# Kernel tuning notes

Measured on AMD Instinct MI355X. Metric: run time of the kernel, lower is better.

Reference implementation:

```python
import jax, jax.numpy as jnp
import numpy as np

T, B, D, A = 512, 64, 1024, 128
NL = 2
AIN = A + 2 * D        # adapt LSTM input size: adapt + x + alstm hidden
PSZ = 2 * D + 12 * D   # policy size per layer (bias=True): ninp+nhid + 12*nhid


def setup_inputs() -> dict:
    key = jax.random.key(0)
    ks = jax.random.split(key, 12)
    r = lambda k, s: jax.random.normal(k, s, dtype=jnp.float32) * 0.03
    return {
        "x": jax.random.normal(ks[0], (T, B, D), dtype=jnp.float32),
        # layer 0
        "a_wih0": r(ks[1], (4 * A, AIN)), "a_whh0": r(ks[2], (4 * A, A)),
        "a_bih0": jnp.zeros((4 * A,), jnp.float32), "a_bhh0": jnp.zeros((4 * A,), jnp.float32),
        "p_w0": r(ks[3], (PSZ, A)), "p_b0": jnp.ones((PSZ,), jnp.float32),
        "f_wih0": r(ks[4], (4 * D, D)), "f_whh0": r(ks[5], (4 * D, D)),
        "f_b0": jnp.zeros((4 * D,), jnp.float32),
        # layer 1
        "a_wih1": r(ks[6], (4 * A, AIN)), "a_whh1": r(ks[7], (4 * A, A)),
        "a_bih1": jnp.zeros((4 * A,), jnp.float32), "a_bhh1": jnp.zeros((4 * A,), jnp.float32),
        "p_w1": r(ks[8], (PSZ, A)), "p_b1": jnp.ones((PSZ,), jnp.float32),
        "f_wih1": r(ks[9], (4 * D, D)), "f_whh1": r(ks[10], (4 * D, D)),
        "f_b1": jnp.zeros((4 * D,), jnp.float32),
    }


def _lstm_cell(x, h, c, wih, whh, bih, bhh):
    g = x @ wih.T + bih + h @ whh.T + bhh      # [B, 4A]
    i, f, gg, o = jnp.split(g, 4, axis=1)
    c2 = jax.nn.sigmoid(f) * c + jax.nn.sigmoid(i) * jnp.tanh(gg)
    h2 = jax.nn.sigmoid(o) * jnp.tanh(c2)
    return h2, c2


def _alstm_cell(xt, h, c, pol, wih, whh, b):
    # policy chunks: [ninp, nhid, 4n, 4n, 4n] with ninp=nhid=D
    p0 = pol[:, :D]
    p1 = pol[:, D:2 * D]
    p2 = pol[:, 2 * D:6 * D]
    p3 = pol[:, 6 * D:10 * D]
    p4 = pol[:, 10 * D:14 * D]
    ig = ((xt * p0) @ wih.T) * p2 + b * p4
    hg = ((h * p1) @ whh.T) * p3
    g = ig + hg
    i, f, gg, o = jnp.split(g, 4, axis=1)
    c2 = jax.nn.sigmoid(f) * c + jax.nn.sigmoid(i) * jnp.tanh(gg)
    h2 = jax.nn.sigmoid(o) * jnp.tanh(c2)
    return h2, c2


def reference(x, a_wih0, a_whh0, a_bih0, a_bhh0, p_w0, p_b0, f_wih0, f_whh0, f_b0,
              a_wih1, a_whh1, a_bih1, a_bhh1, p_w1, p_b1, f_wih1, f_whh1, f_b1):
    params = [
        (a_wih0, a_whh0, a_bih0, a_bhh0, p_w0, p_b0, f_wih0, f_whh0, f_b0),
        (a_wih1, a_whh1, a_bih1, a_bhh1, p_w1, p_b1, f_wih1, f_whh1, f_b1),
    ]

    def step(carry, xt):
        ah, ac, fh, fc = (list(t) for t in carry)
        xc = xt
        for l in range(NL):
            awih, awhh, abih, abhh, pw, pb, fwih, fwhh, fb = params[l]
            # nlayers != 1: adapt input = [x, alstm hidden, prev-layer adapt hidden]
            # (Python negative indexing at l=0 picks last layer's adapt hidden from t-1,
            #  matching the torch in-place list update semantics.)
            ax = jnp.concatenate([xc, fh[l], ah[l - 1]], axis=1)
            ah[l], ac[l] = _lstm_cell(ax, ah[l], ac[l], awih, awhh, abih, abhh)
            pol = ah[l] @ pw.T + pb                      # Project: Linear(A -> PSZ)
            fh[l], fc[l] = _alstm_cell(xc, fh[l], fc[l], pol, fwih, fwhh, fb)
            xc = fh[l]
        return (tuple(ah), tuple(ac), tuple(fh), tuple(fc)), xc

    za = jnp.zeros((B, A), x.dtype)
    zf = jnp.zeros((B, D), x.dtype)
    carry0 = ((za,) * NL, (za,) * NL, (zf,) * NL, (zf,) * NL)
    _, ys = jax.lax.scan(step, carry0, x)   # [T, B, D]
    return ys
```

## Files before the change

kernel.cpp:

```cpp
#include <hip/hip_runtime.h>

#define T_ 512
#define B_ 64
#define D_ 1024
#define A_ 128
#define KCAT_ 2304
#define PSZ_ 14336

typedef __attribute__((ext_vector_type(8))) short short8;
typedef __attribute__((ext_vector_type(4))) short short4_t;
typedef __attribute__((ext_vector_type(4))) float float4_t;

__device__ __forceinline__ float sigf(float x){ return 1.0f/(1.0f + __expf(-x)); }
__device__ __forceinline__ float tanhf_(float x){ return 2.0f/(1.0f + __expf(-2.0f*x)) - 1.0f; }

__device__ __forceinline__ short f2bf(float f){
  unsigned u = __builtin_bit_cast(unsigned, f);
  u += 0x7fffu + ((u >> 16) & 1u);
  return (short)(u >> 16);
}
__device__ __forceinline__ float bf2f(short s){
  unsigned u = ((unsigned)(unsigned short)s) << 16;
  return __builtin_bit_cast(float, u);
}

__global__ __launch_bounds__(256) void pk_cat(const float* __restrict__ wih,
                                              const float* __restrict__ whh,
                                              short* __restrict__ dst){
  int c = blockIdx.x*256 + threadIdx.x;
  int n = blockIdx.y;
  if (c >= KCAT_) return;
  float v = (c < 2176) ? wih[(size_t)n*2176 + c] : whh[n*A_ + (c - 2176)];
  dst[(size_t)n*KCAT_ + c] = f2bf(v);
}
__global__ __launch_bounds__(256) void pk_conv(const float* __restrict__ src,
                                               short* __restrict__ dst, int n){
  int i = blockIdx.x*256 + threadIdx.x;
  if (i < n) dst[i] = f2bf(src[i]);
}

__global__ __launch_bounds__(64) void k1_gates(
    const short* __restrict__ Wcat,
    const float* __restrict__ xf,
    const short* __restrict__ xbf,
    const short* __restrict__ fhbf,
    const short* __restrict__ ahp,
    const short* __restrict__ ahs,
    const float* __restrict__ bih, const float* __restrict__ bhh,
    float* __restrict__ gates)
{
  const int lane = threadIdx.x;
  const int mt = blockIdx.x >> 2, nt = blockIdx.x & 3;
  const int row = lane & 15, quad = lane >> 4;
  const int m0 = mt*16;
  const short* wrow = Wcat + (size_t)(m0 + row)*KCAT_ + quad*8;
  const int bq = nt*16 + row;
  float4_t acc = {0.f,0.f,0.f,0.f};

  if (xf){
    const float* xp = xf + (size_t)bq*D_ + quad*8;
    #pragma unroll 4
    for (int ks = 0; ks < 32; ++ks){
      short8 a = *(const short8*)(wrow + ks*32);
      float4_t x0 = *(const float4_t*)(xp + ks*32);
      float4_t x1 = *(const float4_t*)(xp + ks*32 + 4);
      short8 bfr;
      #pragma unroll
      for (int i = 0; i < 4; ++i){ bfr[i] = f2bf(x0[i]); bfr[4+i] = f2bf(x1[i]); }
      acc = __builtin_amdgcn_mfma_f32_16x16x32_bf16(a, bfr, acc, 0, 0, 0);
    }
  } else {
    const short* xp = xbf + (size_t)bq*D_ + quad*8;
    #pragma unroll 4
    for (int ks = 0; ks < 32; ++ks){
      short8 a = *(const short8*)(wrow + ks*32);
      short8 bfr = *(const short8*)(xp + ks*32);
      acc = __builtin_amdgcn_mfma_f32_16x16x32_bf16(a, bfr, acc, 0, 0, 0);
    }
  }
  {
    const short* hp = fhbf + (size_t)bq*D_ + quad*8;
    #pragma unroll 4
    for (int ks = 0; ks < 32; ++ks){
      short8 a = *(const short8*)(wrow + 1024 + ks*32);
      short8 bfr = *(const short8*)(hp + ks*32);
      acc = __builtin_amdgcn_mfma_f32_16x16x32_bf16(a, bfr, acc, 0, 0, 0);
    }
  }
  {
    const short* pp = ahp + bq*A_ + quad*8;
    #pragma unroll
    for (int ks = 0; ks < 4; ++ks){
      short8 a = *(const short8*)(wrow + 2048 + ks*32);
      short8 bfr = *(const short8*)(pp + ks*32);
      acc = __builtin_amdgcn_mfma_f32_16x16x32_bf16(a, bfr, acc, 0, 0, 0);
    }
  }
  {
    const short* sp = ahs + bq*A_ + quad*8;
    #pragma unroll
    for (int ks = 0; ks < 4; ++ks){
      short8 a = *(const short8*)(wrow + 2176 + ks*32);
      short8 bfr = *(const short8*)(sp + ks*32);
      acc = __builtin_amdgcn_mfma_f32_16x16x32_bf16(a, bfr, acc, 0, 0, 0);
    }
  }
  const int b = nt*16 + row;
  const int n0 = m0 + quad*4;
  #pragma unroll
  for (int r = 0; r < 4; ++r){
    int n = n0 + r;
    gates[n*B_ + b] = acc[r] + bih[n] + bhh[n];
  }
}

__global__ __launch_bounds__(256) void k2_cellpol(
    const float* __restrict__ gates,
    const float* __restrict__ ac_old, float* __restrict__ ac_new,
    short* __restrict__ ah_out,
    const short* __restrict__ pwbf,
    const float* __restrict__ pb,
    const float* __restrict__ xf,
    const short* __restrict__ xbf,
    const short* __restrict__ fhbf,
    float* __restrict__ polp,
    short* __restrict__ xp0, short* __restrict__ hp1)
{
  __shared__ short ah_s[64*136];
  const int tid = threadIdx.x;
  const int b = tid & 63, q = tid >> 6;
  for (int jj = 0; jj < 32; ++jj){
    int j = q*32 + jj;
    float gi = gates[(j      )*B_ + b];
    float gf = gates[(j + 128)*B_ + b];
    float gg = gates[(j + 256)*B_ + b];
    float go = gates[(j + 384)*B_ + b];
    float c  = ac_old[j*B_ + b];
    float c2 = sigf(gf)*c + sigf(gi)*tanhf_(gg);
    float h2 = sigf(go)*tanhf_(c2);
    ah_s[b*136 + j] = f2bf(h2);
    if (blockIdx.x == 0){
      ac_new[j*B_ + b] = c2;
      ah_out[b*A_ + j] = f2bf(h2);
    }
  }
  __syncthreads();
  const int lane = tid & 63;
  const int row = lane & 15, quad = lane >> 4;
  const int m0 = (blockIdx.x*4 + q)*16;
  const short* wrow = pwbf + (size_t)(m0 + row)*A_ + quad*8;
  float4_t acc[4] = {{0.f,0.f,0.f,0.f},{0.f,0.f,0.f,0.f},{0.f,0.f,0.f,0.f},{0.f,0.f,0.f,0.f}};
  #pragma unroll
  for (int ks = 0; ks < 4; ++ks){
    short8 a = *(const short8*)(wrow + ks*32);
    #pragma unroll
    for (int nt = 0; nt < 4; ++nt){
      short8 bf8 = *(const short8*)&ah_s[(nt*16 + row)*136 + ks*32 + quad*8];
      acc[nt] = __builtin_amdgcn_mfma_f32_16x16x32_bf16(a, bf8, acc[nt], 0, 0, 0);
    }
  }
  const int c0 = m0 + quad*4;
  float4_t pbv = *(const float4_t*)(pb + c0);
  if (m0 < 1024){
    #pragma unroll
    for (int nt = 0; nt < 4; ++nt){
      int b2 = nt*16 + row;
      float4_t xv;
      if (xf){ xv = *(const float4_t*)(xf + (size_t)b2*D_ + c0); }
      else {
        short4_t xb = *(const short4_t*)(xbf + (size_t)b2*D_ + c0);
        #pragma unroll
        for (int r = 0; r < 4; ++r) xv[r] = bf2f(xb[r]);
      }
      short4_t o;
      #pragma unroll
      for (int r = 0; r < 4; ++r) o[r] = f2bf((acc[nt][r] + pbv[r]) * xv[r]);
      *(short4_t*)(xp0 + (size_t)b2*D_ + c0) = o;
    }
  } else if (m0 < 2048){
    int cc = c0 - 1024;
    #pragma unroll
    for (int nt = 0; nt < 4; ++nt){
      int b2 = nt*16 + row;
      short4_t hb = *(const short4_t*)(fhbf + (size_t)b2*D_ + cc);
      short4_t o;
      #pragma unroll
      for (int r = 0; r < 4; ++r) o[r] = f2bf((acc[nt][r] + pbv[r]) * bf2f(hb[r]));
      *(short4_t*)(hp1 + (size_t)b2*D_ + cc) = o;
    }
  } else {
    int cc = c0 - 2048;
    #pragma unroll
    for (int nt = 0; nt < 4; ++nt){
      int b2 = nt*16 + row;
      float4_t vv;
      #pragma unroll
      for (int r = 0; r < 4; ++r) vv[r] = acc[nt][r] + pbv[r];
      *(float4_t*)(polp + (size_t)b2*12288 + cc) = vv;
    }
  }
}

__global__ __launch_bounds__(256) void k3_fast(
    const short* __restrict__ wI,
    const short* __restrict__ wH,
    const short* __restrict__ xp0, const short* __restrict__ hp1,
    const float* __restrict__ polp,
    const float* __restrict__ fb,
    float* __restrict__ fc,
    short* __restrict__ fhbf,
    float* __restrict__ outp)
{
  const int tid = threadIdx.x;
  const int lane = tid & 63, nt = tid >> 6;
  const int row = lane & 15, quad = lane >> 4;
  const int j0 = blockIdx.x*16;
  const short* wIr[4]; const short* wHr[4];
  #pragma unroll
  for (int g = 0; g < 4; ++g){
    wIr[g] = wI + (size_t)(g*D_ + j0 + row)*D_ + quad*8;
    wHr[g] = wH + (size_t)(g*D_ + j0 + row)*D_ + quad*8;
  }
  const short* bx = xp0 + (size_t)(nt*16 + row)*D_ + quad*8;
  const short* bh = hp1 + (size_t)(nt*16 + row)*D_ + quad*8;
  float4_t aI[4] = {{0.f,0.f,0.f,0.f},{0.f,0.f,0.f,0.f},{0.f,0.f,0.f,0.f},{0.f,0.f,0.f,0.f}};
  float4_t aH[4] = {{0.f,0.f,0.f,0.f},{0.f,0.f,0.f,0.f},{0.f,0.f,0.f,0.f},{0.f,0.f,0.f,0.f}};
  #pragma unroll 2
  for (int ks = 0; ks < 32; ++ks){
    const int kg = ks*32;
    short8 bxf = *(const short8*)(bx + kg);
    short8 bhf = *(const short8*)(bh + kg);
    #pragma unroll
    for (int g = 0; g < 4; ++g){
      short8 ai = *(const short8*)(wIr[g] + kg);
      short8 ah = *(const short8*)(wHr[g] + kg);
      aI[g] = __builtin_amdgcn_mfma_f32_16x16x32_bf16(ai, bxf, aI[g], 0, 0, 0);
      aH[g] = __builtin_amdgcn_mfma_f32_16x16x32_bf16(ah, bhf, aH[g], 0, 0, 0);
    }
  }
  const int b = nt*16 + row;
  const int jr = j0 + quad*4;
  float4_t gl[4];
  #pragma unroll
  for (int g = 0; g < 4; ++g){
    const float* pbase = polp + (size_t)b*12288 + g*D_ + jr;
    float4_t p2 = *(const float4_t*)(pbase);
    float4_t p3 = *(const float4_t*)(pbase + 4096);
    float4_t p4 = *(const float4_t*)(pbase + 8192);
    float4_t fbv = *(const float4_t*)(fb + g*D_ + jr);
    #pragma unroll
    for (int r = 0; r < 4; ++r)
      gl[g][r] = aI[g][r]*p2[r] + fbv[r]*p4[r] + aH[g][r]*p3[r];
  }
  float4_t cold = *(const float4_t*)(fc + (size_t)b*D_ + jr);
  float4_t cnew, hnew;
  #pragma unroll
  for (int r = 0; r < 4; ++r){
    float c2 = sigf(gl[1][r])*cold[r] + sigf(gl[0][r])*tanhf_(gl[2][r]);
    float h2 = sigf(gl[3][r])*tanhf_(c2);
    cnew[r] = c2; hnew[r] = h2;
  }
  *(float4_t*)(fc + (size_t)b*D_ + jr) = cnew;
  short4_t hb;
  #pragma unroll
  for (int r = 0; r < 4; ++r) hb[r] = f2bf(hnew[r]);
  *(short4_t*)(fhbf + (size_t)b*D_ + jr) = hb;
  if (outp) *(float4_t*)(outp + (size_t)b*D_ + jr) = hnew;
}

extern "C" void kernel_launch(void* const* d_in, const int* in_sizes, int n_in,
                              void* d_out, int out_size, void* d_ws, size_t ws_size,
                              hipStream_t stream) {
  const float* x = (const float*)d_in[0];
  const float* a_wih[2] = {(const float*)d_in[1],  (const float*)d_in[10]};
  const float* a_whh[2] = {(const float*)d_in[2],  (const float*)d_in[11]};
  const float* a_bih[2] = {(const float*)d_in[3],  (const float*)d_in[12]};
  const float* a_bhh[2] = {(const float*)d_in[4],  (const float*)d_in[13]};
  const float* p_w[2]   = {(const float*)d_in[5],  (const float*)d_in[14]};
  const float* p_b[2]   = {(const float*)d_in[6],  (const float*)d_in[15]};
  const float* f_wih[2] = {(const float*)d_in[7],  (const float*)d_in[16]};
  const float* f_whh[2] = {(const float*)d_in[8],  (const float*)d_in[17]};
  const float* f_b[2]   = {(const float*)d_in[9],  (const float*)d_in[18]};

  char* w = (char*)d_ws;
  float* gates = (float*)(w + 0);
  float* ac    = (float*)(w + 131072);
  float* fc    = (float*)(w + 262144);
  float* polp  = (float*)(w + 786432);
  short* xp0   = (short*)(w + 3932160);
  short* hp1   = (short*)(w + 4063232);
  short* fhbf  = (short*)(w + 4194304);
  short* ahbf  = (short*)(w + 4456448);
  short* Wcat  = (short*)(w + 4521984);
  short* pwbf  = (short*)(w + 9240576);
  short* fwihb = (short*)(w + 16580608);
  short* fwhhb = (short*)(w + 33357824);

  hipMemsetAsync(w + 131072, 0, 655360, stream);
  hipMemsetAsync(w + 4194304, 0, 327680, stream);

  for (int l = 0; l < 2; ++l){
    pk_cat<<<dim3(9,512), 256, 0, stream>>>(a_wih[l], a_whh[l], Wcat + (size_t)l*512*KCAT_);
    pk_conv<<<(PSZ_*A_ + 255)/256, 256, 0, stream>>>(p_w[l], pwbf + (size_t)l*PSZ_*A_, PSZ_*A_);
    pk_conv<<<(4*D_*D_ + 255)/256, 256, 0, stream>>>(f_wih[l], fwihb + (size_t)l*4*D_*D_, 4*D_*D_);
    pk_conv<<<(4*D_*D_ + 255)/256, 256, 0, stream>>>(f_whh[l], fwhhb + (size_t)l*4*D_*D_, 4*D_*D_);
  }

  for (int t = 0; t < T_; ++t){
    const int par = t & 1, cur = par ^ 1;
    const float* xt = x + (size_t)t*B_*D_;
    for (int l = 0; l < 2; ++l){
      const float* xf  = (l == 0) ? xt : nullptr;
      const short* xbf = fhbf;
      const short* fh_l = fhbf + (size_t)l*B_*D_;
      const short* ahp = (l == 0) ? ahbf + (1*2 + par)*B_*A_
                                  : ahbf + (0*2 + cur)*B_*A_;
      const short* ahs = ahbf + (l*2 + par)*B_*A_;
      short* ah_out    = ahbf + (l*2 + cur)*B_*A_;
      const float* ac_old = ac + (l*2 + par)*A_*B_;
      float* ac_new       = ac + (l*2 + cur)*A_*B_;

      k1_gates<<<128, 64, 0, stream>>>(
          Wcat + (size_t)l*512*KCAT_, xf, xbf, fh_l, ahp, ahs,
          a_bih[l], a_bhh[l], gates);

      k2_cellpol<<<224, 256, 0, stream>>>(
          gates, ac_old, ac_new, ah_out,
          pwbf + (size_t)l*PSZ_*A_, p_b[l], xf, xbf, fh_l,
          polp, xp0, hp1);

      k3_fast<<<64, 256, 0, stream>>>(
          fwihb + (size_t)l*4*D_*D_, fwhhb + (size_t)l*4*D_*D_,
          xp0, hp1, polp, f_b[l],
          fc + (size_t)l*B_*D_, (short*)fh_l,
          (l == 1) ? (float*)d_out + (size_t)t*B_*D_ : nullptr);
    }
  }
}
```

Before: 87.29 ms.

## Fuse per-step kernels into one persistent kernel with grid-wide barriers

Replaces 3072 small kernel launches (three kernels per layer per timestep) with a single persistent kernel of 256 blocks. The kernel loops over time and layers and separates the stages with an atomic-counter grid barrier. The gate GEMM also splits its K dimension across four wavefronts per block and reduces the partial sums in shared memory. This removes launch and inter-kernel gaps, at the cost of barrier spin latency and the requirement that all 256 blocks are resident at the same time.

```diff
diff --git a/kernel.cpp b/kernel.cpp
--- a/kernel.cpp
+++ b/kernel.cpp
@@ -6,6 +6,7 @@
 #define A_ 128
 #define KCAT_ 2304
 #define PSZ_ 14336
+#define NBLK 256
 
 typedef __attribute__((ext_vector_type(8))) short short8;
 typedef __attribute__((ext_vector_type(4))) short short4_t;
@@ -39,233 +40,263 @@
   if (i < n) dst[i] = f2bf(src[i]);
 }
 
-__global__ __launch_bounds__(64) void k1_gates(
-    const short* __restrict__ Wcat,
-    const float* __restrict__ xf,
-    const short* __restrict__ xbf,
-    const short* __restrict__ fhbf,
-    const short* __restrict__ ahp,
-    const short* __restrict__ ahs,
-    const float* __restrict__ bih, const float* __restrict__ bhh,
-    float* __restrict__ gates)
-{
-  const int lane = threadIdx.x;
-  const int mt = blockIdx.x >> 2, nt = blockIdx.x & 3;
-  const int row = lane & 15, quad = lane >> 4;
-  const int m0 = mt*16;
-  const short* wrow = Wcat + (size_t)(m0 + row)*KCAT_ + quad*8;
-  const int bq = nt*16 + row;
-  float4_t acc = {0.f,0.f,0.f,0.f};
-
-  if (xf){
-    const float* xp = xf + (size_t)bq*D_ + quad*8;
-    #pragma unroll 4
-    for (int ks = 0; ks < 32; ++ks){
-      short8 a = *(const short8*)(wrow + ks*32);
-      float4_t x0 = *(const float4_t*)(xp + ks*32);
-      float4_t x1 = *(const float4_t*)(xp + ks*32 + 4);
-      short8 bfr;
-      #pragma unroll
-      for (int i = 0; i < 4; ++i){ bfr[i] = f2bf(x0[i]); bfr[4+i] = f2bf(x1[i]); }
-      acc = __builtin_amdgcn_mfma_f32_16x16x32_bf16(a, bfr, acc, 0, 0, 0);
-    }
-  } else {
-    const short* xp = xbf + (size_t)bq*D_ + quad*8;
-    #pragma unroll 4
-    for (int ks = 0; ks < 32; ++ks){
-      short8 a = *(const short8*)(wrow + ks*32);
-      short8 bfr = *(const short8*)(xp + ks*32);
-      acc = __builtin_amdgcn_mfma_f32_16x16x32_bf16(a, bfr, acc, 0, 0, 0);
+struct Args {
+  const float* x;
+  const short* Wcat0; const short* Wcat1;
+  const float* bih0;  const float* bih1;
+  const float* bhh0;  const float* bhh1;
+  const short* pw0;   const short* pw1;
+  const float* pb0;   const float* pb1;
+  const short* fwi0;  const short* fwi1;
+  const short* fwh0;  const short* fwh1;
+  const float* fb0;   const float* fb1;
+  float* gates; float* ac; float* fc; float* polp;
+  short* xp0; short* hp1; short* fhbf; short* ahbf;
+  float* out;
+  unsigned* bar;
+};
+
+__device__ __forceinline__ void gsync(unsigned* bar, unsigned target){
+  __syncthreads();
+  if (threadIdx.x == 0){
+    __threadfence();
+    __hip_atomic_fetch_add(bar, 1u, __ATOMIC_RELAXED, __HIP_MEMORY_SCOPE_AGENT);
+    while (__hip_atomic_load(bar, __ATOMIC_RELAXED, __HIP_MEMORY_SCOPE_AGENT) < target)
+      __builtin_amdgcn_s_sleep(2);
+    __threadfence();
+  }
+  __syncthreads();
+}
+
+__global__ __launch_bounds__(256, 1) void fused(Args P){
+  const int tid  = threadIdx.x;
+  const int blk  = blockIdx.x;
+  const int wq   = tid >> 6;
+  const int lane = tid & 63;
+  const int row  = lane & 15, quad = lane >> 4;
+
+  __shared__ float red[4][256];
+  __shared__ short ah_s[64*136];
+
+  unsigned ph = 0;
+
+  for (int t = 0; t < T_; ++t){
+    const int par = t & 1, cur = par ^ 1;
+    const float* xt = P.x + (size_t)t*B_*D_;
+    #pragma unroll
+    for (int l = 0; l < 2; ++l){
+      const short* Wcat = l ? P.Wcat1 : P.Wcat0;
+      const float* bih  = l ? P.bih1  : P.bih0;
+      const float* bhh  = l ? P.bhh1  : P.bhh0;
+      const short* pw   = l ? P.pw1   : P.pw0;
+      const float* pb   = l ? P.pb1   : P.pb0;
+      const short* fwi  = l ? P.fwi1  : P.fwi0;
+      const short* fwh  = l ? P.fwh1  : P.fwh0;
+      const float* fb   = l ? P.fb1   : P.fb0;
+      short* fh_l = P.fhbf + (size_t)l*B_*D_;
+      const short* ahp = l ? (P.ahbf + (0*2 + cur)*B_*A_)
+                           : (P.ahbf + (1*2 + par)*B_*A_);
+      const short* ahs = P.ahbf + (l*2 + par)*B_*A_;
+      short* ah_out    = P.ahbf + (l*2 + cur)*B_*A_;
+      const float* ac_old = P.ac + (l*2 + par)*A_*B_;
+      float* ac_new       = P.ac + (l*2 + cur)*A_*B_;
+      float* fc_l = P.fc + (size_t)l*B_*D_;
+
+      if (blk < 128){
+        const int m0  = (blk >> 2) * 16;
+        const int nt1 = blk & 3;
+        const int bq  = nt1*16 + row;
+        const short* wrow = Wcat + (size_t)(m0 + row)*KCAT_ + quad*8;
+        float4_t acc = {0.f,0.f,0.f,0.f};
+        if (l == 0){
+          const float* xp = xt + (size_t)bq*D_ + quad*8;
+          #pragma unroll
+          for (int i = 0; i < 8; ++i){
+            const int ks = wq + 4*i;
+            short8 a = *(const short8*)(wrow + ks*32);
+            float4_t x0 = *(const float4_t*)(xp + ks*32);
+            float4_t x1 = *(const float4_t*)(xp + ks*32 + 4);
+            short8 bfr;
+            #pragma unroll
+            for (int r = 0; r < 4; ++r){ bfr[r] = f2bf(x0[r]); bfr[4+r] = f2bf(x1[r]); }
+            acc = __builtin_amdgcn_mfma_f32_16x16x32_bf16(a, bfr, acc, 0, 0, 0);
+          }
+        } else {
+          const short* xp = P.fhbf + (size_t)bq*D_ + quad*8;
+          #pragma unroll
+          for (int i = 0; i < 8; ++i){
+            const int ks = wq + 4*i;
+            short8 a = *(const short8*)(wrow + ks*32);
+            short8 bfr = *(const short8*)(xp + ks*32);
+            acc = __builtin_amdgcn_mfma_f32_16x16x32_bf16(a, bfr, acc, 0, 0, 0);
+          }
+        }
+        {
+          const short* hp = fh_l + (size_t)bq*D_ + quad*8;
+          #pragma unroll
+          for (int i = 0; i < 8; ++i){
+            const int ks = wq + 4*i;
+            short8 a = *(const short8*)(wrow + 1024 + ks*32);
+            short8 bfr = *(const short8*)(hp + ks*32);
+            acc = __builtin_amdgcn_mfma_f32_16x16x32_bf16(a, bfr, acc, 0, 0, 0);
+          }
+        }
+        {
+          short8 a = *(const short8*)(wrow + 2048 + wq*32);
+          short8 bfr = *(const short8*)(ahp + bq*A_ + quad*8 + wq*32);
+          acc = __builtin_amdgcn_mfma_f32_16x16x32_bf16(a, bfr, acc, 0, 0, 0);
+        }
+        {
+          short8 a = *(const short8*)(wrow + 2176 + wq*32);
+          short8 bfr = *(const short8*)(ahs + bq*A_ + quad*8 + wq*32);
+          acc = __builtin_amdgcn_mfma_f32_16x16x32_bf16(a, bfr, acc, 0, 0, 0);
+        }
+        #pragma unroll
+        for (int r = 0; r < 4; ++r) red[wq][(r << 6) | lane] = acc[r];
+        __syncthreads();
+        {
+          float s = red[0][tid] + red[1][tid] + red[2][tid] + red[3][tid];
+          const int rr = tid >> 6, ll = tid & 63;
+          const int n = m0 + ((ll >> 4) << 2) + rr;
+          const int b = nt1*16 + (ll & 15);
+          P.gates[n*B_ + b] = s + bih[n] + bhh[n];
+        }
+      }
+      gsync(P.bar, ++ph * NBLK);
+
+      if (blk < 224){
+        const int b = tid & 63, q = tid >> 6;
+        #pragma unroll 4
+        for (int jj = 0; jj < 32; ++jj){
+          const int j = q*32 + jj;
+          float gi = P.gates[(j      )*B_ + b];
+          float gf = P.gates[(j + 128)*B_ + b];
+          float gg = P.gates[(j + 256)*B_ + b];
+          float go = P.gates[(j + 384)*B_ + b];
+          float c  = ac_old[j*B_ + b];
+          float c2 = sigf(gf)*c + sigf(gi)*tanhf_(gg);
+          float h2 = sigf(go)*tanhf_(c2);
+          ah_s[b*136 + j] = f2bf(h2);
+          if (blk == 0){
+            ac_new[j*B_ + b] = c2;
+            ah_out[b*A_ + j] = f2bf(h2);
+          }
+        }
+        __syncthreads();
+        const int m0 = (blk*4 + wq)*16;
+        const short* wrow = pw + (size_t)(m0 + row)*A_ + quad*8;
+        float4_t acc[4] = {{0.f,0.f,0.f,0.f},{0.f,0.f,0.f,0.f},{0.f,0.f,0.f,0.f},{0.f,0.f,0.f,0.f}};
+        #pragma unroll
+        for (int ks = 0; ks < 4; ++ks){
+          short8 a = *(const short8*)(wrow + ks*32);
+          #pragma unroll
+          for (int nt = 0; nt < 4; ++nt){
+            short8 bf8 = *(const short8*)&ah_s[(nt*16 + row)*136 + ks*32 + quad*8];
+            acc[nt] = __builtin_amdgcn_mfma_f32_16x16x32_bf16(a, bf8, acc[nt], 0, 0, 0);
+          }
+        }
+        const int c0 = m0 + quad*4;
+        float4_t pbv = *(const float4_t*)(pb + c0);
+        if (m0 < 1024){
+          #pragma unroll
+          for (int nt = 0; nt < 4; ++nt){
+            const int b2 = nt*16 + row;
+            float4_t xv;
+            if (l == 0){ xv = *(const float4_t*)(xt + (size_t)b2*D_ + c0); }
+            else {
+              short4_t xb = *(const short4_t*)(P.fhbf + (size_t)b2*D_ + c0);
+              #pragma unroll
+              for (int r = 0; r < 4; ++r) xv[r] = bf2f(xb[r]);
+            }
+            short4_t o;
+            #pragma unroll
+            for (int r = 0; r < 4; ++r) o[r] = f2bf((acc[nt][r] + pbv[r]) * xv[r]);
+            *(short4_t*)(P.xp0 + (size_t)b2*D_ + c0) = o;
+          }
+        } else if (m0 < 2048){
+          const int cc = c0 - 1024;
+          #pragma unroll
+          for (int nt = 0; nt < 4; ++nt){
+            const int b2 = nt*16 + row;
+            short4_t hb = *(const short4_t*)(fh_l + (size_t)b2*D_ + cc);
+            short4_t o;
+            #pragma unroll
+            for (int r = 0; r < 4; ++r) o[r] = f2bf((acc[nt][r] + pbv[r]) * bf2f(hb[r]));
+            *(short4_t*)(P.hp1 + (size_t)b2*D_ + cc) = o;
+          }
+        } else {
+          const int cc = c0 - 2048;
+          #pragma unroll
+          for (int nt = 0; nt < 4; ++nt){
+            const int b2 = nt*16 + row;
+            float4_t vv;
+            #pragma unroll
+            for (int r = 0; r < 4; ++r) vv[r] = acc[nt][r] + pbv[r];
+            *(float4_t*)(P.polp + (size_t)b2*12288 + cc) = vv;
+          }
+        }
+      }
+      gsync(P.bar, ++ph * NBLK);
+
+      if (blk < 64){
+        const int nt3 = wq;
+        const int j0 = blk*16;
+        const short* wIr[4]; const short* wHr[4];
+        #pragma unroll
+        for (int g = 0; g < 4; ++g){
+          wIr[g] = fwi + (size_t)(g*D_ + j0 + row)*D_ + quad*8;
+          wHr[g] = fwh + (size_t)(g*D_ + j0 + row)*D_ + quad*8;
+        }
+        const short* bx = P.xp0 + (size_t)(nt3*16 + row)*D_ + quad*8;
+        const short* bh = P.hp1 + (size_t)(nt3*16 + row)*D_ + quad*8;
+        float4_t aI[4] = {{0.f,0.f,0.f,0.f},{0.f,0.f,0.f,0.f},{0.f,0.f,0.f,0.f},{0.f,0.f,0.f,0.f}};
+        float4_t aH[4] = {{0.f,0.f,0.f,0.f},{0.f,0.f,0.f,0.f},{0.f,0.f,0.f,0.f},{0.f,0.f,0.f,0.f}};
+        #pragma unroll 2
+        for (int ks = 0; ks < 32; ++ks){
+          const int kg = ks*32;
+          short8 bxf = *(const short8*)(bx + kg);
+          short8 bhf = *(const short8*)(bh + kg);
+          #pragma unroll
+          for (int g = 0; g < 4; ++g){
+            short8 ai  = *(const short8*)(wIr[g] + kg);
+            short8 ah8 = *(const short8*)(wHr[g] + kg);
+            aI[g] = __builtin_amdgcn_mfma_f32_16x16x32_bf16(ai,  bxf, aI[g], 0, 0, 0);
+            aH[g] = __builtin_amdgcn_mfma_f32_16x16x32_bf16(ah8, bhf, aH[g], 0, 0, 0);
+          }
+        }
+        const int b3 = nt3*16 + row;
+        const int jr = j0 + quad*4;
+        float4_t gl[4];
+        #pragma unroll
+        for (int g = 0; g < 4; ++g){
+          const float* pbase = P.polp + (size_t)b3*12288 + g*D_ + jr;
+          float4_t p2 = *(const float4_t*)(pbase);
+          float4_t p3 = *(const float4_t*)(pbase + 4096);
+          float4_t p4 = *(const float4_t*)(pbase + 8192);
+          float4_t fbv = *(const float4_t*)(fb + g*D_ + jr);
+          #pragma unroll
+          for (int r = 0; r < 4; ++r)
+            gl[g][r] = aI[g][r]*p2[r] + fbv[r]*p4[r] + aH[g][r]*p3[r];
+        }
+        float4_t cold = *(const float4_t*)(fc_l + (size_t)b3*D_ + jr);
+        float4_t cnew, hnew;
+        #pragma unroll
+        for (int r = 0; r < 4; ++r){
+          float c2 = sigf(gl[1][r])*cold[r] + sigf(gl[0][r])*tanhf_(gl[2][r]);
+          float h2 = sigf(gl[3][r])*tanhf_(c2);
+          cnew[r] = c2; hnew[r] = h2;
+        }
+        *(float4_t*)(fc_l + (size_t)b3*D_ + jr) = cnew;
+        short4_t hb;
+        #pragma unroll
+        for (int r = 0; r < 4; ++r) hb[r] = f2bf(hnew[r]);
+        *(short4_t*)(fh_l + (size_t)b3*D_ + jr) = hb;
+        if (l == 1)
+          *(float4_t*)(P.out + (size_t)t*B_*D_ + (size_t)b3*D_ + jr) = hnew;
+      }
+      gsync(P.bar, ++ph * NBLK);
     }
   }
-  {
-    const short* hp = fhbf + (size_t)bq*D_ + quad*8;
-    #pragma unroll 4
-    for (int ks = 0; ks < 32; ++ks){
-      short8 a = *(const short8*)(wrow + 1024 + ks*32);
-      short8 bfr = *(const short8*)(hp + ks*32);
-      acc = __builtin_amdgcn_mfma_f32_16x16x32_bf16(a, bfr, acc, 0, 0, 0);
-    }
-  }
-  {
-    const short* pp = ahp + bq*A_ + quad*8;
-    #pragma unroll
-    for (int ks = 0; ks < 4; ++ks){
-      short8 a = *(const short8*)(wrow + 2048 + ks*32);
-      short8 bfr = *(const short8*)(pp + ks*32);
-      acc = __builtin_amdgcn_mfma_f32_16x16x32_bf16(a, bfr, acc, 0, 0, 0);
-    }
-  }
-  {
-    const short* sp = ahs + bq*A_ + quad*8;
-    #pragma unroll
-    for (int ks = 0; ks < 4; ++ks){
-      short8 a = *(const short8*)(wrow + 2176 + ks*32);
-      short8 bfr = *(const short8*)(sp + ks*32);
-      acc = __builtin_amdgcn_mfma_f32_16x16x32_bf16(a, bfr, acc, 0, 0, 0);
-    }
-  }
-  const int b = nt*16 + row;
-  const int n0 = m0 + quad*4;
-  #pragma unroll
-  for (int r = 0; r < 4; ++r){
-    int n = n0 + r;
-    gates[n*B_ + b] = acc[r] + bih[n] + bhh[n];
-  }
-}
-
-__global__ __launch_bounds__(256) void k2_cellpol(
-    const float* __restrict__ gates,
-    const float* __restrict__ ac_old, float* __restrict__ ac_new,
-    short* __restrict__ ah_out,
-    const short* __restrict__ pwbf,
-    const float* __restrict__ pb,
-    const float* __restrict__ xf,
-    const short* __restrict__ xbf,
-    const short* __restrict__ fhbf,
-    float* __restrict__ polp,
-    short* __restrict__ xp0, short* __restrict__ hp1)
-{
-  __shared__ short ah_s[64*136];
-  const int tid = threadIdx.x;
-  const int b = tid & 63, q = tid >> 6;
-  for (int jj = 0; jj < 32; ++jj){
-    int j = q*32 + jj;
-    float gi = gates[(j      )*B_ + b];
-    float gf = gates[(j + 128)*B_ + b];
-    float gg = gates[(j + 256)*B_ + b];
-    float go = gates[(j + 384)*B_ + b];
-    float c  = ac_old[j*B_ + b];
-    float c2 = sigf(gf)*c + sigf(gi)*tanhf_(gg);
-    float h2 = sigf(go)*tanhf_(c2);
-    ah_s[b*136 + j] = f2bf(h2);
-    if (blockIdx.x == 0){
-      ac_new[j*B_ + b] = c2;
-      ah_out[b*A_ + j] = f2bf(h2);
-    }
-  }
-  __syncthreads();
-  const int lane = tid & 63;
-  const int row = lane & 15, quad = lane >> 4;
-  const int m0 = (blockIdx.x*4 + q)*16;
-  const short* wrow = pwbf + (size_t)(m0 + row)*A_ + quad*8;
-  float4_t acc[4] = {{0.f,0.f,0.f,0.f},{0.f,0.f,0.f,0.f},{0.f,0.f,0.f,0.f},{0.f,0.f,0.f,0.f}};
-  #pragma unroll
-  for (int ks = 0; ks < 4; ++ks){
-    short8 a = *(const short8*)(wrow + ks*32);
-    #pragma unroll
-    for (int nt = 0; nt < 4; ++nt){
-      short8 bf8 = *(const short8*)&ah_s[(nt*16 + row)*136 + ks*32 + quad*8];
-      acc[nt] = __builtin_amdgcn_mfma_f32_16x16x32_bf16(a, bf8, acc[nt], 0, 0, 0);
-    }
-  }
-  const int c0 = m0 + quad*4;
-  float4_t pbv = *(const float4_t*)(pb + c0);
-  if (m0 < 1024){
-    #pragma unroll
-    for (int nt = 0; nt < 4; ++nt){
-      int b2 = nt*16 + row;
-      float4_t xv;
-      if (xf){ xv = *(const float4_t*)(xf + (size_t)b2*D_ + c0); }
-      else {
-        short4_t xb = *(const short4_t*)(xbf + (size_t)b2*D_ + c0);
-        #pragma unroll
-        for (int r = 0; r < 4; ++r) xv[r] = bf2f(xb[r]);
-      }
-      short4_t o;
-      #pragma unroll
-      for (int r = 0; r < 4; ++r) o[r] = f2bf((acc[nt][r] + pbv[r]) * xv[r]);
-      *(short4_t*)(xp0 + (size_t)b2*D_ + c0) = o;
-    }
-  } else if (m0 < 2048){
-    int cc = c0 - 1024;
-    #pragma unroll
-    for (int nt = 0; nt < 4; ++nt){
-      int b2 = nt*16 + row;
-      short4_t hb = *(const short4_t*)(fhbf + (size_t)b2*D_ + cc);
-      short4_t o;
-      #pragma unroll
-      for (int r = 0; r < 4; ++r) o[r] = f2bf((acc[nt][r] + pbv[r]) * bf2f(hb[r]));
-      *(short4_t*)(hp1 + (size_t)b2*D_ + cc) = o;
-    }
-  } else {
-    int cc = c0 - 2048;
-    #pragma unroll
-    for (int nt = 0; nt < 4; ++nt){
-      int b2 = nt*16 + row;
-      float4_t vv;
-      #pragma unroll
-      for (int r = 0; r < 4; ++r) vv[r] = acc[nt][r] + pbv[r];
-      *(float4_t*)(polp + (size_t)b2*12288 + cc) = vv;
-    }
-  }
-}
-
-__global__ __launch_bounds__(256) void k3_fast(
-    const short* __restrict__ wI,
-    const short* __restrict__ wH,
-    const short* __restrict__ xp0, const short* __restrict__ hp1,
-    const float* __restrict__ polp,
-    const float* __restrict__ fb,
-    float* __restrict__ fc,
-    short* __restrict__ fhbf,
-    float* __restrict__ outp)
-{
-  const int tid = threadIdx.x;
-  const int lane = tid & 63, nt = tid >> 6;
-  const int row = lane & 15, quad = lane >> 4;
-  const int j0 = blockIdx.x*16;
-  const short* wIr[4]; const short* wHr[4];
-  #pragma unroll
-  for (int g = 0; g < 4; ++g){
-    wIr[g] = wI + (size_t)(g*D_ + j0 + row)*D_ + quad*8;
-    wHr[g] = wH + (size_t)(g*D_ + j0 + row)*D_ + quad*8;
-  }
-  const short* bx = xp0 + (size_t)(nt*16 + row)*D_ + quad*8;
-  const short* bh = hp1 + (size_t)(nt*16 + row)*D_ + quad*8;
-  float4_t aI[4] = {{0.f,0.f,0.f,0.f},{0.f,0.f,0.f,0.f},{0.f,0.f,0.f,0.f},{0.f,0.f,0.f,0.f}};
-  float4_t aH[4] = {{0.f,0.f,0.f,0.f},{0.f,0.f,0.f,0.f},{0.f,0.f,0.f,0.f},{0.f,0.f,0.f,0.f}};
-  #pragma unroll 2
-  for (int ks = 0; ks < 32; ++ks){
-    const int kg = ks*32;
-    short8 bxf = *(const short8*)(bx + kg);
-    short8 bhf = *(const short8*)(bh + kg);
-    #pragma unroll
-    for (int g = 0; g < 4; ++g){
-      short8 ai = *(const short8*)(wIr[g] + kg);
-      short8 ah = *(const short8*)(wHr[g] + kg);
-      aI[g] = __builtin_amdgcn_mfma_f32_16x16x32_bf16(ai, bxf, aI[g], 0, 0, 0);
-      aH[g] = __builtin_amdgcn_mfma_f32_16x16x32_bf16(ah, bhf, aH[g], 0, 0, 0);
-    }
-  }
-  const int b = nt*16 + row;
-  const int jr = j0 + quad*4;
-  float4_t gl[4];
-  #pragma unroll
-  for (int g = 0; g < 4; ++g){
-    const float* pbase = polp + (size_t)b*12288 + g*D_ + jr;
-    float4_t p2 = *(const float4_t*)(pbase);
-    float4_t p3 = *(const float4_t*)(pbase + 4096);
-    float4_t p4 = *(const float4_t*)(pbase + 8192);
-    float4_t fbv = *(const float4_t*)(fb + g*D_ + jr);
-    #pragma unroll
-    for (int r = 0; r < 4; ++r)
-      gl[g][r] = aI[g][r]*p2[r] + fbv[r]*p4[r] + aH[g][r]*p3[r];
-  }
-  float4_t cold = *(const float4_t*)(fc + (size_t)b*D_ + jr);
-  float4_t cnew, hnew;
-  #pragma unroll
-  for (int r = 0; r < 4; ++r){
-    float c2 = sigf(gl[1][r])*cold[r] + sigf(gl[0][r])*tanhf_(gl[2][r]);
-    float h2 = sigf(gl[3][r])*tanhf_(c2);
-    cnew[r] = c2; hnew[r] = h2;
-  }
-  *(float4_t*)(fc + (size_t)b*D_ + jr) = cnew;
-  short4_t hb;
-  #pragma unroll
-  for (int r = 0; r < 4; ++r) hb[r] = f2bf(hnew[r]);
-  *(short4_t*)(fhbf + (size_t)b*D_ + jr) = hb;
-  if (outp) *(float4_t*)(outp + (size_t)b*D_ + jr) = hnew;
 }
 
 extern "C" void kernel_launch(void* const* d_in, const int* in_sizes, int n_in,
@@ -295,9 +326,11 @@
   short* pwbf  = (short*)(w + 9240576);
   short* fwihb = (short*)(w + 16580608);
   short* fwhhb = (short*)(w + 33357824);
+  unsigned* bar = (unsigned*)(w + 50135040);
 
   hipMemsetAsync(w + 131072, 0, 655360, stream);
   hipMemsetAsync(w + 4194304, 0, 327680, stream);
+  hipMemsetAsync(w + 50135040, 0, 64, stream);
 
   for (int l = 0; l < 2; ++l){
     pk_cat<<<dim3(9,512), 256, 0, stream>>>(a_wih[l], a_whh[l], Wcat + (size_t)l*512*KCAT_);
@@ -306,34 +339,20 @@
     pk_conv<<<(4*D_*D_ + 255)/256, 256, 0, stream>>>(f_whh[l], fwhhb + (size_t)l*4*D_*D_, 4*D_*D_);
   }
 
-  for (int t = 0; t < T_; ++t){
-    const int par = t & 1, cur = par ^ 1;
-    const float* xt = x + (size_t)t*B_*D_;
-    for (int l = 0; l < 2; ++l){
-      const float* xf  = (l == 0) ? xt : nullptr;
-      const short* xbf = fhbf;
-      const short* fh_l = fhbf + (size_t)l*B_*D_;
-      const short* ahp = (l == 0) ? ahbf + (1*2 + par)*B_*A_
-                                  : ahbf + (0*2 + cur)*B_*A_;
-      const short* ahs = ahbf + (l*2 + par)*B_*A_;
-      short* ah_out    = ahbf + (l*2 + cur)*B_*A_;
-      const float* ac_old = ac + (l*2 + par)*A_*B_;
-      float* ac_new       = ac + (l*2 + cur)*A_*B_;
-
-      k1_gates<<<128, 64, 0, stream>>>(
-          Wcat + (size_t)l*512*KCAT_, xf, xbf, fh_l, ahp, ahs,
-          a_bih[l], a_bhh[l], gates);
-
-      k2_cellpol<<<224, 256, 0, stream>>>(
-          gates, ac_old, ac_new, ah_out,
-          pwbf + (size_t)l*PSZ_*A_, p_b[l], xf, xbf, fh_l,
-          polp, xp0, hp1);
-
-      k3_fast<<<64, 256, 0, stream>>>(
-          fwihb + (size_t)l*4*D_*D_, fwhhb + (size_t)l*4*D_*D_,
-          xp0, hp1, polp, f_b[l],
-          fc + (size_t)l*B_*D_, (short*)fh_l,
-          (l == 1) ? (float*)d_out + (size_t)t*B_*D_ : nullptr);
-    }
-  }
-}
+  Args A;
+  A.x = x;
+  A.Wcat0 = Wcat;  A.Wcat1 = Wcat + (size_t)512*KCAT_;
+  A.bih0 = a_bih[0]; A.bih1 = a_bih[1];
+  A.bhh0 = a_bhh[0]; A.bhh1 = a_bhh[1];
+  A.pw0 = pwbf;    A.pw1 = pwbf + (size_t)PSZ_*A_;
+  A.pb0 = p_b[0];  A.pb1 = p_b[1];
+  A.fwi0 = fwihb;  A.fwi1 = fwihb + (size_t)4*D_*D_;
+  A.fwh0 = fwhhb;  A.fwh1 = fwhhb + (size_t)4*D_*D_;
+  A.fb0 = f_b[0];  A.fb1 = f_b[1];
+  A.gates = gates; A.ac = ac; A.fc = fc; A.polp = polp;
+  A.xp0 = xp0; A.hp1 = hp1; A.fhbf = fhbf; A.ahbf = ahbf;
+  A.out = (float*)d_out;
+  A.bar = bar;
+
+  fused<<<NBLK, 256, 0, stream>>>(A);
+}
```

Measured after the change: 137.1 ms. +57.1%, slower.
